# Performance work log

Measured on AMD Instinct MI355X. Metric: run time of the kernel, lower is better.

## Reference

```python
import jax, jax.numpy as jnp
import numpy as np

B, T, H = 64, 2048, 64  # basins, daily timesteps, MLP hidden width


def _mlp(x, W1, b1, W2, b2, W3, b3, W4, b4):
    # x: [..., 4] -> [..., 5]; tanh hidden layers, linear head
    h = jnp.tanh(x @ W1 + b1)
    h = jnp.tanh(h @ W2 + b2)
    h = jnp.tanh(h @ W3 + b3)
    return h @ W4 + b4


def _step(x):
    # smooth step function from the torch module
    return (jnp.tanh(5.0 * x) + 1.0) * 0.5


def _interp(series, t):
    # linear interpolation of per-basin forcing series [B, T] at scalar time t
    # (time grid is the integer daily grid 0..T-1, matching time_series)
    n = series.shape[1]
    i0 = jnp.clip(jnp.floor(t).astype(jnp.int32), 0, n - 2)
    frac = t - i0.astype(series.dtype)
    pair = jax.lax.dynamic_slice_in_dim(series, i0, 2, axis=1)  # [B, 2]
    return pair[:, 0] * (1.0 - frac) + pair[:, 1] * frac


def _forward(s_snow, s_water, precp_series, tmean_series, lday_series, time_series,
             W1, b1, W2, b2, W3, b3, W4, b4):
    params = (W1, b1, W2, b2, W3, b3, W4, b4)

    def rhs(t, y):  # y: [B, 2]
        s0, s1 = y[:, 0], y[:, 1]
        precp = _interp(precp_series, t)
        temp = _interp(tmean_series, t)
        lday = _interp(lday_series, t)
        o = _mlp(jnp.stack([s0, s1, precp, temp], axis=-1), *params)  # [B, 5]
        # scale_target_vars=True branch
        p_snow = jax.nn.relu(jnp.sinh(o[:, 0]) * _step(-temp))
        p_rain = jax.nn.relu(jnp.sinh(o[:, 1]))
        m = jax.nn.relu(_step(s0) * jnp.sinh(o[:, 2]))
        et = _step(s1) * jnp.exp(o[:, 3]) * lday
        q = _step(s1) * jnp.exp(o[:, 4])
        return jnp.stack([p_snow - m, p_rain + m - et - q], axis=-1)

    y0 = jnp.stack([s_snow[:, 0], s_water[:, 0]], axis=-1)  # [B, 2]
    t0s = time_series[:-1]
    dts = time_series[1:] - time_series[:-1]

    def scan_step(y, td):  # classic RK4 between consecutive grid points
        t0, dt = td
        half = dt * 0.5
        k1 = rhs(t0, y)
        k2 = rhs(t0 + half, y + half * k1)
        k3 = rhs(t0 + half, y + half * k2)
        k4 = rhs(t0 + dt, y + dt * k3)
        y_next = y + (dt / 6.0) * (k1 + 2.0 * k2 + 2.0 * k3 + k4)
        return y_next, y_next

    _, ys = jax.lax.scan(scan_step, y0, (t0s, dts))  # [T-1, B, 2]
    y_full = jnp.concatenate([y0[None], ys], axis=0)  # [T, B, 2]
    y_full = jnp.transpose(y_full, (1, 0, 2))  # [B, T, 2]

    # final NN pass over the integrated states + raw forcing series
    inputs_nn = jnp.stack(
        [y_full[..., 0], y_full[..., 1], precp_series, tmean_series], axis=-1)  # [B, T, 4]
    q_out = _mlp(inputs_nn, *params)[..., -1]  # [B, T] (last output column = q)
    return q_out


def setup_inputs() -> dict:
    key = jax.random.key(0)
    ks = jax.random.split(key, 9)
    return {
        "s_snow": jax.random.uniform(ks[0], (B, T), dtype=jnp.float32),
        "s_water": jax.random.uniform(ks[1], (B, T), dtype=jnp.float32),
        "precp_series": jax.random.uniform(ks[2], (B, T), dtype=jnp.float32),
        "tmean_series": jax.random.normal(ks[3], (B, T), dtype=jnp.float32),
        "lday_series": jax.random.uniform(ks[4], (B, T), dtype=jnp.float32) * 0.5,
        "time_series": jnp.arange(T, dtype=jnp.float32),
        "W1": jax.random.normal(ks[5], (4, H), dtype=jnp.float32) / jnp.sqrt(4.0),
        "b1": jnp.zeros((H,), jnp.float32),
        "W2": jax.random.normal(ks[6], (H, H), dtype=jnp.float32) / jnp.sqrt(float(H)),
        "b2": jnp.zeros((H,), jnp.float32),
        "W3": jax.random.normal(ks[7], (H, H), dtype=jnp.float32) / jnp.sqrt(float(H)),
        "b3": jnp.zeros((H,), jnp.float32),
        "W4": jax.random.normal(ks[8], (H, 5), dtype=jnp.float32) * (0.1 / jnp.sqrt(float(H))),
        "b4": jnp.zeros((5,), jnp.float32),
    }


def reference(s_snow, s_water, precp_series, tmean_series, lday_series, time_series,
              W1, b1, W2, b2, W3, b3, W4, b4):
    return _forward(s_snow, s_water, precp_series, tmean_series, lday_series,
                    time_series, W1, b1, W2, b2, W3, b3, W4, b4)
```

## Files before the change

kernel.cpp:

```cpp
#include <hip/hip_runtime.h>
#include <cmath>

#define LOG2E 1.44269504088896340736f
#define TMAX 2048

#if __has_builtin(__builtin_amdgcn_exp2f)
#define EXP2F(x) __builtin_amdgcn_exp2f(x)
#else
#define EXP2F(x) exp2f(x)
#endif
#if __has_builtin(__builtin_amdgcn_rcpf)
#define RCPF(x) __builtin_amdgcn_rcpf(x)
#else
#define RCPF(x) (1.0f / (x))
#endif

typedef float float2v __attribute__((ext_vector_type(2)));
typedef float float4v __attribute__((ext_vector_type(4)));

__device__ __forceinline__ float fexp(float x)  { return EXP2F(x * LOG2E); }
__device__ __forceinline__ float ftanh(float x) { return 1.0f - 2.0f * RCPF(1.0f + EXP2F(x * (2.0f * LOG2E))); }
__device__ __forceinline__ float fstep(float x) { return RCPF(1.0f + EXP2F(x * (-10.0f * LOG2E))); }
__device__ __forceinline__ float fsinh(float x) { float e = fexp(x); return 0.5f * (e - RCPF(e)); }

__device__ __forceinline__ int fadd_i(int a, int b) {
    return __builtin_bit_cast(int, __builtin_bit_cast(float, a) + __builtin_bit_cast(float, b));
}

__device__ __forceinline__ float wave_sum63(float x) {
    int v = __builtin_bit_cast(int, x);
    v = fadd_i(v, __builtin_amdgcn_update_dpp(0, v, 0x111, 0xF, 0xF, true));
    v = fadd_i(v, __builtin_amdgcn_update_dpp(0, v, 0x112, 0xF, 0xF, true));
    v = fadd_i(v, __builtin_amdgcn_update_dpp(0, v, 0x114, 0xF, 0xF, true));
    v = fadd_i(v, __builtin_amdgcn_update_dpp(0, v, 0x118, 0xF, 0xF, true));
    v = fadd_i(v, __builtin_amdgcn_update_dpp(0, v, 0x142, 0xA, 0xF, true));
    v = fadd_i(v, __builtin_amdgcn_update_dpp(0, v, 0x143, 0xC, 0xF, true));
    return __builtin_bit_cast(float, v);
}

__device__ __forceinline__ float2v pk_fma(float2v a, float2v b, float2v c) {
    float2v d;
    asm("v_pk_fma_f32 %0, %1, %2, %3" : "=v"(d) : "v"(a), "v"(b), "v"(c));
    return d;
}

__device__ __forceinline__ float2v vlo(float4v v) { return __builtin_shufflevector(v, v, 0, 1); }
__device__ __forceinline__ float2v vhi(float4v v) { return __builtin_shufflevector(v, v, 2, 3); }

__global__ __launch_bounds__(256, 1)
void exphydro_kernel(const float* __restrict__ g_snow, const float* __restrict__ g_water,
                     const float* __restrict__ g_pr, const float* __restrict__ g_tm,
                     const float* __restrict__ g_ld, const float* __restrict__ g_t,
                     const float* __restrict__ W1, const float* __restrict__ b1,
                     const float* __restrict__ W2, const float* __restrict__ b2,
                     const float* __restrict__ W3, const float* __restrict__ b3,
                     const float* __restrict__ W4, const float* __restrict__ b4,
                     float* __restrict__ out, int T)
{
    const int tid  = threadIdx.x;
    const int lane = tid & 63;
    const int wid  = tid >> 6;
    const int b    = blockIdx.x;

    __shared__ __align__(16) float4v s_f[TMAX];
    __shared__ __align__(16) float hcopy[4][64];
    __shared__ __align__(16) float partA[64][4];
    __shared__ __align__(16) float partB[64][4];
    __shared__ __align__(16) float obuf[8];

    for (int i = tid; i < T; i += 256) {
        s_f[i] = float4v{g_pr[b * T + i], g_tm[b * T + i], g_ld[b * T + i], g_t[i]};
    }

    float w1r[4];
#pragma unroll
    for (int j = 0; j < 4; ++j) w1r[j] = W1[j * 64 + lane];
    float b1v = b1[lane];

    float2v w2s[8], w3s[8];
#pragma unroll
    for (int k = 0; k < 8; ++k) {
        int r = 16 * wid + 2 * k;
        w2s[k] = float2v{W2[r * 64 + lane], W2[(r + 1) * 64 + lane]};
        w3s[k] = float2v{W3[r * 64 + lane], W3[(r + 1) * 64 + lane]};
    }
    float b2v = (wid == 0) ? b2[lane] : 0.0f;
    float b3v = (wid == 0) ? b3[lane] : 0.0f;
    float w4a = W4[lane * 5 + wid];
    float w4b = (wid == 3) ? W4[lane * 5 + 4] : 0.0f;
    float b4a = b4[wid];
    float b4b = b4[4];

    __syncthreads();

    auto quarter_dot = [&](const float* hq, const float2v (&w)[8], float bias) -> float {
        float4v q0 = *reinterpret_cast<const float4v*>(hq + 0);
        float4v q1 = *reinterpret_cast<const float4v*>(hq + 4);
        float4v q2 = *reinterpret_cast<const float4v*>(hq + 8);
        float4v q3 = *reinterpret_cast<const float4v*>(hq + 12);
        float2v a0 = float2v{bias, 0.0f}, a1 = float2v{0.0f, 0.0f};
        a0 = pk_fma(w[0], vlo(q0), a0); a1 = pk_fma(w[1], vhi(q0), a1);
        a0 = pk_fma(w[2], vlo(q1), a0); a1 = pk_fma(w[3], vhi(q1), a1);
        a0 = pk_fma(w[4], vlo(q2), a0); a1 = pk_fma(w[5], vhi(q2), a1);
        a0 = pk_fma(w[6], vlo(q3), a0); a1 = pk_fma(w[7], vhi(q3), a1);
        float2v s = a0 + a1;
        return s.x + s.y;
    };

    auto mlp_obuf = [&](float h1) {
        float* hown = &hcopy[wid][0];
        const float* hq = hown + 16 * wid;
        hown[lane] = h1;
        partA[lane][wid] = quarter_dot(hq, w2s, b2v);
        __syncthreads();
        float4v p2 = *reinterpret_cast<const float4v*>(&partA[lane][0]);
        float h2 = ftanh((p2.x + p2.y) + (p2.z + p2.w));
        hown[lane] = h2;
        partB[lane][wid] = quarter_dot(hq, w3s, b3v);
        __syncthreads();
        float4v p3 = *reinterpret_cast<const float4v*>(&partB[lane][0]);
        float h3 = ftanh((p3.x + p3.y) + (p3.z + p3.w));
        float t1 = wave_sum63(w4a * h3);
        if (wid == 3) {
            float t2 = wave_sum63(w4b * h3);
            if (lane == 63) { obuf[3] = t1 + b4a; obuf[4] = t2 + b4b; }
        } else {
            if (lane == 63) obuf[wid] = t1 + b4a;
        }
        __syncthreads();
    };

    auto rhs = [&](float base, float y0v, float y1v, float ld, float snt,
                   float& d0, float& d1, float& o4) {
        float h1 = ftanh(fmaf(w1r[0], y0v, fmaf(w1r[1], y1v, base)));
        mlp_obuf(h1);
        float4v ov = *reinterpret_cast<const float4v*>(&obuf[0]);
        float o4v = obuf[4];
        float psnow = fmaxf(0.0f, fsinh(ov.x) * snt);
        float prain = fmaxf(0.0f, fsinh(ov.y));
        float melt  = fmaxf(0.0f, fstep(y0v) * fsinh(ov.z));
        float eq    = fstep(y1v) * fmaf(fexp(ov.w), ld, fexp(o4v));
        d0 = psnow - melt;
        d1 = (prain + melt) - eq;
        o4 = o4v;
    };

    float y0v = g_snow[b * T];
    float y1v = g_water[b * T];

    for (int st = 0; st < T - 1; ++st) {
        float4v fc = s_f[st];
        float4v fn = s_f[st + 1];

        float dt = fn.w - fc.w, half = 0.5f * dt, c6 = dt * (1.0f / 6.0f);
        float prH = 0.5f * (fc.x + fn.x);
        float tmH = 0.5f * (fc.y + fn.y);
        float ldH = 0.5f * (fc.z + fn.z);
        float snA = fstep(-fc.y), snH = fstep(-tmH), snC = fstep(-fn.y);
        float baseA = fmaf(w1r[2], fc.x, fmaf(w1r[3], fc.y, b1v));
        float baseH = fmaf(w1r[2], prH,  fmaf(w1r[3], tmH,  b1v));
        float baseC = fmaf(w1r[2], fn.x, fmaf(w1r[3], fn.y, b1v));

        float k1a, k1b, k2a, k2b, k3a, k3b, k4a, k4b, o4a, o4x;
        rhs(baseA, y0v, y1v, fc.z, snA, k1a, k1b, o4a);
        if (tid == 0) out[b * T + st] = o4a;
        rhs(baseH, fmaf(half, k1a, y0v), fmaf(half, k1b, y1v), ldH, snH, k2a, k2b, o4x);
        rhs(baseH, fmaf(half, k2a, y0v), fmaf(half, k2b, y1v), ldH, snH, k3a, k3b, o4x);
        rhs(baseC, fmaf(dt, k3a, y0v),   fmaf(dt, k3b, y1v),   fn.z, snC, k4a, k4b, o4x);

        y0v = fmaf(c6, (k1a + k4a) + 2.0f * (k2a + k3a), y0v);
        y1v = fmaf(c6, (k1b + k4b) + 2.0f * (k2b + k3b), y1v);
    }

    {
        float4v fL = s_f[T - 1];
        float base = fmaf(w1r[2], fL.x, fmaf(w1r[3], fL.y, b1v));
        float h1 = ftanh(fmaf(w1r[0], y0v, fmaf(w1r[1], y1v, base)));
        mlp_obuf(h1);
        if (tid == 0) out[b * T + (T - 1)] = obuf[4];
    }
}

extern "C" void kernel_launch(void* const* d_in, const int* in_sizes, int n_in,
                              void* d_out, int out_size, void* d_ws, size_t ws_size,
                              hipStream_t stream) {
    const float* g_snow  = (const float*)d_in[0];
    const float* g_water = (const float*)d_in[1];
    const float* g_pr    = (const float*)d_in[2];
    const float* g_tm    = (const float*)d_in[3];
    const float* g_ld    = (const float*)d_in[4];
    const float* g_t     = (const float*)d_in[5];
    const float* W1 = (const float*)d_in[6];
    const float* b1 = (const float*)d_in[7];
    const float* W2 = (const float*)d_in[8];
    const float* b2 = (const float*)d_in[9];
    const float* W3 = (const float*)d_in[10];
    const float* b3 = (const float*)d_in[11];
    const float* W4 = (const float*)d_in[12];
    const float* b4 = (const float*)d_in[13];

    const int T = in_sizes[5];
    const int B = in_sizes[0] / T;

    exphydro_kernel<<<dim3(B), dim3(256), 0, stream>>>(
        g_snow, g_water, g_pr, g_tm, g_ld, g_t,
        W1, b1, W2, b2, W3, b3, W4, b4,
        (float*)d_out, T);
}
```

Baseline: 5.921 ms.

## Compute all MLP outputs redundantly per wave to drop final barrier

Each wave now loads all five W4 columns and reduces all five output dot products itself with DPP reductions. The result is broadcast to the wave with readlane from lane 63, so the shared obuf and the third __syncthreads per RHS evaluation are gone. The partial-sum buffers are also transposed to [wave][lane], which trades one vector LDS load for four scalar loads in exchange for conflict-free writes. The cost is more redundant reduction work per wave in this latency-bound serial loop.

New measurement: 5.845 ms. About the same (-1.3%).

```diff
diff --git a/kernel.cpp b/kernel.cpp
--- a/kernel.cpp
+++ b/kernel.cpp
@@ -36,6 +36,10 @@
     v = fadd_i(v, __builtin_amdgcn_update_dpp(0, v, 0x142, 0xA, 0xF, true));
     v = fadd_i(v, __builtin_amdgcn_update_dpp(0, v, 0x143, 0xC, 0xF, true));
     return __builtin_bit_cast(float, v);
+}
+
+__device__ __forceinline__ float rl(float x, int l) {
+    return __builtin_bit_cast(float, __builtin_amdgcn_readlane(__builtin_bit_cast(int, x), l));
 }
 
 __device__ __forceinline__ float2v pk_fma(float2v a, float2v b, float2v c) {
@@ -64,9 +68,8 @@
 
     __shared__ __align__(16) float4v s_f[TMAX];
     __shared__ __align__(16) float hcopy[4][64];
-    __shared__ __align__(16) float partA[64][4];
-    __shared__ __align__(16) float partB[64][4];
-    __shared__ __align__(16) float obuf[8];
+    __shared__ __align__(16) float partA[4][64];
+    __shared__ __align__(16) float partB[4][64];
 
     for (int i = tid; i < T; i += 256) {
         s_f[i] = float4v{g_pr[b * T + i], g_tm[b * T + i], g_ld[b * T + i], g_t[i]};
@@ -86,10 +89,9 @@
     }
     float b2v = (wid == 0) ? b2[lane] : 0.0f;
     float b3v = (wid == 0) ? b3[lane] : 0.0f;
-    float w4a = W4[lane * 5 + wid];
-    float w4b = (wid == 3) ? W4[lane * 5 + 4] : 0.0f;
-    float b4a = b4[wid];
-    float b4b = b4[4];
+    float w4r[5], b4r[5];
+#pragma unroll
+    for (int k = 0; k < 5; ++k) { w4r[k] = W4[lane * 5 + k]; b4r[k] = b4[k]; }
 
     __syncthreads();
 
@@ -107,42 +109,35 @@
         return s.x + s.y;
     };
 
-    auto mlp_obuf = [&](float h1) {
+    auto mlp_o63 = [&](float h1, float* o) {
         float* hown = &hcopy[wid][0];
         const float* hq = hown + 16 * wid;
         hown[lane] = h1;
-        partA[lane][wid] = quarter_dot(hq, w2s, b2v);
+        partA[wid][lane] = quarter_dot(hq, w2s, b2v);
         __syncthreads();
-        float4v p2 = *reinterpret_cast<const float4v*>(&partA[lane][0]);
-        float h2 = ftanh((p2.x + p2.y) + (p2.z + p2.w));
+        float h2 = ftanh((partA[0][lane] + partA[1][lane]) + (partA[2][lane] + partA[3][lane]));
         hown[lane] = h2;
-        partB[lane][wid] = quarter_dot(hq, w3s, b3v);
+        partB[wid][lane] = quarter_dot(hq, w3s, b3v);
         __syncthreads();
-        float4v p3 = *reinterpret_cast<const float4v*>(&partB[lane][0]);
-        float h3 = ftanh((p3.x + p3.y) + (p3.z + p3.w));
-        float t1 = wave_sum63(w4a * h3);
-        if (wid == 3) {
-            float t2 = wave_sum63(w4b * h3);
-            if (lane == 63) { obuf[3] = t1 + b4a; obuf[4] = t2 + b4b; }
-        } else {
-            if (lane == 63) obuf[wid] = t1 + b4a;
-        }
-        __syncthreads();
+        float h3 = ftanh((partB[0][lane] + partB[1][lane]) + (partB[2][lane] + partB[3][lane]));
+#pragma unroll
+        for (int k = 0; k < 5; ++k) o[k] = wave_sum63(w4r[k] * h3) + b4r[k];
     };
 
     auto rhs = [&](float base, float y0v, float y1v, float ld, float snt,
                    float& d0, float& d1, float& o4) {
         float h1 = ftanh(fmaf(w1r[0], y0v, fmaf(w1r[1], y1v, base)));
-        mlp_obuf(h1);
-        float4v ov = *reinterpret_cast<const float4v*>(&obuf[0]);
-        float o4v = obuf[4];
-        float psnow = fmaxf(0.0f, fsinh(ov.x) * snt);
-        float prain = fmaxf(0.0f, fsinh(ov.y));
-        float melt  = fmaxf(0.0f, fstep(y0v) * fsinh(ov.z));
-        float eq    = fstep(y1v) * fmaf(fexp(ov.w), ld, fexp(o4v));
-        d0 = psnow - melt;
-        d1 = (prain + melt) - eq;
-        o4 = o4v;
+        float o[5];
+        mlp_o63(h1, o);
+        float psnow = fmaxf(0.0f, fsinh(o[0]) * snt);
+        float prain = fmaxf(0.0f, fsinh(o[1]));
+        float melt  = fmaxf(0.0f, fstep(y0v) * fsinh(o[2]));
+        float eq    = fstep(y1v) * fmaf(fexp(o[3]), ld, fexp(o[4]));
+        float d0l = psnow - melt;
+        float d1l = (prain + melt) - eq;
+        d0 = rl(d0l, 63);
+        d1 = rl(d1l, 63);
+        o4 = o[4];
     };
 
     float y0v = g_snow[b * T];
@@ -163,7 +158,7 @@
 
         float k1a, k1b, k2a, k2b, k3a, k3b, k4a, k4b, o4a, o4x;
         rhs(baseA, y0v, y1v, fc.z, snA, k1a, k1b, o4a);
-        if (tid == 0) out[b * T + st] = o4a;
+        if (tid == 63) out[b * T + st] = o4a;
         rhs(baseH, fmaf(half, k1a, y0v), fmaf(half, k1b, y1v), ldH, snH, k2a, k2b, o4x);
         rhs(baseH, fmaf(half, k2a, y0v), fmaf(half, k2b, y1v), ldH, snH, k3a, k3b, o4x);
         rhs(baseC, fmaf(dt, k3a, y0v),   fmaf(dt, k3b, y1v),   fn.z, snC, k4a, k4b, o4x);
@@ -176,8 +171,9 @@
         float4v fL = s_f[T - 1];
         float base = fmaf(w1r[2], fL.x, fmaf(w1r[3], fL.y, b1v));
         float h1 = ftanh(fmaf(w1r[0], y0v, fmaf(w1r[1], y1v, base)));
-        mlp_obuf(h1);
-        if (tid == 0) out[b * T + (T - 1)] = obuf[4];
+        float o[5];
+        mlp_o63(h1, o);
+        if (tid == 63) out[b * T + (T - 1)] = o[4];
     }
 }
 
```
